# Optimization experiments

Hardware: AMD Instinct MI355X
Metric: run time of the kernel (lower is better)

Reference implementation:

```python
import jax, jax.numpy as jnp
import numpy as np

EPS = 1e-5
L = 8      # n_layers
H = 1024   # n_hidden
F_IN = 26  # input features
B = 65536  # batch


def layer_norm(x, gamma, beta):
    m = jnp.mean(x, axis=-1, keepdims=True)
    v = jnp.mean((x - m) ** 2, axis=-1, keepdims=True)
    return (x - m) * jax.lax.rsqrt(v + EPS) * gamma + beta


def setup_inputs() -> dict:
    key = jax.random.key(0)
    ks = jax.random.split(key, 12)
    s_in = 1.0 / np.sqrt(F_IN)
    s_h = 1.0 / np.sqrt(H)
    return {
        "x": jax.random.normal(ks[0], (B, F_IN), jnp.float32),
        "st_gamma": jnp.ones((F_IN,), jnp.float32),
        "st_beta": jnp.zeros((F_IN,), jnp.float32),
        "st_w": jax.random.uniform(ks[1], (H, F_IN), jnp.float32, -s_in, s_in),
        "st_b": jax.random.uniform(ks[2], (H,), jnp.float32, -s_in, s_in),
        "blk_gamma": jnp.ones((L, H), jnp.float32),
        "blk_beta": jnp.zeros((L, H), jnp.float32),
        "blk_w": jax.random.uniform(ks[3], (L, H, H), jnp.float32, -s_h, s_h),
        "blk_b": jax.random.uniform(ks[4], (L, H), jnp.float32, -s_h, s_h),
        "last_gamma": jnp.ones((H,), jnp.float32),
        "last_beta": jnp.zeros((H,), jnp.float32),
        "last_w": jax.random.uniform(ks[5], (1, H), jnp.float32, -s_h, s_h),
        "last_b": jax.random.uniform(ks[6], (1,), jnp.float32, -s_h, s_h),
    }


def reference(x, st_gamma, st_beta, st_w, st_b,
              blk_gamma, blk_beta, blk_w, blk_b,
              last_gamma, last_beta, last_w, last_b):
    # Stem: LN(26) -> Linear(26->H) -> ReLU (dropout = identity in eval)
    h = jax.nn.relu(layer_norm(x, st_gamma, st_beta) @ st_w.T + st_b)

    # n_layers blocks: LN -> Linear(H->H) -> ReLU, scanned over stacked params
    def body(h, params):
        g, b, w, bb = params
        h = jax.nn.relu(layer_norm(h, g, b) @ w.T + bb)
        return h, None

    h, _ = jax.lax.scan(body, h, (blk_gamma, blk_beta, blk_w, blk_b))

    # Head: LN -> Linear(H->1) -> sigmoid
    h = layer_norm(h, last_gamma, last_beta)
    out = jax.nn.sigmoid(h @ last_w.T + last_b)  # [B, 1]
    return out
```

## Files before the change

kernel.cpp:

```cpp
#include <hip/hip_runtime.h>
#include <hip/hip_bf16.h>
#include <stdint.h>


typedef __attribute__((ext_vector_type(8))) _Float16 f16x8;
typedef __attribute__((ext_vector_type(4))) float f32x4;

#define EPSLN 1e-5f
#define HDIM 1024

__device__ __forceinline__ void gload16(const void* g, void* l) {
  __builtin_amdgcn_global_load_lds(
      (const __attribute__((address_space(1))) unsigned int*)g,
      (__attribute__((address_space(3))) unsigned int*)l, 16, 0, 0);
}

__global__ __launch_bounds__(256) void zero_f32(float* __restrict__ p, int n) {
  int i = blockIdx.x * 256 + threadIdx.x;
  if (i < n) p[i] = 0.f;
}

__global__ __launch_bounds__(256) void fold_blk(
    const float* __restrict__ bg, const float* __restrict__ bb,
    const float* __restrict__ bw, const float* __restrict__ bbias,
    _Float16* __restrict__ Wf, float* __restrict__ bfold, float* __restrict__ Sfold) {
  int lo = blockIdx.x;
  int layer = lo >> 10;
  const float* wrow = bw + (size_t)lo * HDIM;
  const float* g = bg + (size_t)layer * HDIM;
  const float* be = bb + (size_t)layer * HDIM;
  _Float16* wout = Wf + (size_t)lo * HDIM;
  int t = threadIdx.x;
  float s = 0.f, acb = 0.f;
  for (int i = t; i < HDIM; i += 256) {
    float wv = wrow[i];
    _Float16 wp = (_Float16)(wv * g[i]);
    wout[i] = wp;
    s += (float)wp;
    acb += be[i] * wv;
  }
#pragma unroll
  for (int off = 1; off < 64; off <<= 1) { s += __shfl_xor(s, off); acb += __shfl_xor(acb, off); }
  __shared__ float rs[4], rb[4];
  int l = t & 63, w = t >> 6;
  if (l == 0) { rs[w] = s; rb[w] = acb; }
  __syncthreads();
  if (t == 0) {
    Sfold[lo] = rs[0] + rs[1] + rs[2] + rs[3];
    bfold[lo] = bbias[lo] + rb[0] + rb[1] + rb[2] + rb[3];
  }
}

__global__ __launch_bounds__(256) void fold_head(
    const float* __restrict__ lg, const float* __restrict__ lb,
    const float* __restrict__ lw, const float* __restrict__ lbias,
    float* __restrict__ headW, float* __restrict__ headAux) {
  int t = threadIdx.x;
  float s = 0.f, acb = 0.f;
  for (int i = t; i < HDIM; i += 256) {
    float wp = lw[i] * lg[i];
    headW[i] = wp;
    s += wp;
    acb += lb[i] * lw[i];
  }
#pragma unroll
  for (int off = 1; off < 64; off <<= 1) { s += __shfl_xor(s, off); acb += __shfl_xor(acb, off); }
  __shared__ float rs[4], rb[4];
  int l = t & 63, w = t >> 6;
  if (l == 0) { rs[w] = s; rb[w] = acb; }
  __syncthreads();
  if (t == 0) {
    headAux[0] = rs[0] + rs[1] + rs[2] + rs[3];
    headAux[1] = lbias[0] + rb[0] + rb[1] + rb[2] + rb[3];
  }
}

__global__ __launch_bounds__(256) void fold_stem(const float* __restrict__ stw,
                                                 _Float16* __restrict__ Wst) {
  int idx = blockIdx.x * 256 + threadIdx.x;
  int o = idx >> 6, j = idx & 63;
  int i = (((j >> 3) ^ (o & 7)) << 3) + (j & 7);
  Wst[idx] = (i < 26) ? (_Float16)stw[o * 26 + i] : (_Float16)0.f;
}

__global__ __launch_bounds__(256) void stem_gemm(
    const float* __restrict__ x, const float* __restrict__ stg, const float* __restrict__ stb,
    const _Float16* __restrict__ Wst, const float* __restrict__ stbias,
    _Float16* __restrict__ hout, float* __restrict__ stats_out, int rowBase) {
  __shared__ float xin[128 * 26];
  __shared__ _Float16 As[128 * 64];
  __shared__ _Float16 Bs[128 * 64];
  const int t = threadIdx.x;
  const int l = t & 63;
  const int w = t >> 6;
  const int wm = w >> 1, wn = w & 1;
  const int brow = blockIdx.x * 128;
  const int bcol = blockIdx.y * 128;

  const _Float16* gb = Wst + (size_t)(bcol + (t >> 3)) * 64 + (t & 7) * 8;
  char* lB = (char*)Bs + (size_t)w * 1024;
#pragma unroll
  for (int q = 0; q < 4; ++q) gload16(gb + (size_t)q * 32 * 64, lB + q * 4096);

  const float* src = x + ((size_t)rowBase + brow) * 26;
  for (int i = t; i < 128 * 26; i += 256) xin[i] = src[i];
  __syncthreads();

  if (t < 128) {
    float m = 0.f;
#pragma unroll
    for (int i = 0; i < 26; ++i) m += xin[t * 26 + i];
    m *= (1.f / 26.f);
    float v = 0.f;
#pragma unroll
    for (int i = 0; i < 26; ++i) { float d = xin[t * 26 + i] - m; v += d * d; }
    float rstd = rsqrtf(v * (1.f / 26.f) + EPSLN);
    _Float16 tmp[32];
#pragma unroll
    for (int i = 0; i < 26; ++i)
      tmp[i] = (_Float16)((xin[t * 26 + i] - m) * rstd * stg[i] + stb[i]);
#pragma unroll
    for (int i = 26; i < 32; ++i) tmp[i] = (_Float16)0.f;
    char* arow = (char*)As + t * 128;
#pragma unroll
    for (int c = 0; c < 4; ++c) {
      f16x8 vv;
#pragma unroll
      for (int j = 0; j < 8; ++j) vv[j] = tmp[c * 8 + j];
      *(f16x8*)(arow + ((c ^ (t & 7)) << 4)) = vv;
    }
    f16x8 vz = (f16x8)(_Float16)0.f;
#pragma unroll
    for (int c = 4; c < 8; ++c) *(f16x8*)(arow + ((c ^ (t & 7)) << 4)) = vz;
  }
  __syncthreads();

  f32x4 acc[4][4];
#pragma unroll
  for (int i = 0; i < 4; ++i)
#pragma unroll
    for (int j = 0; j < 4; ++j) acc[i][j] = (f32x4){0.f, 0.f, 0.f, 0.f};

#pragma unroll
  for (int ks = 0; ks < 2; ++ks) {
    const int cx = ((ks * 4 + (l >> 4)) ^ (l & 7)) << 4;
    f16x8 af[4], bfr[4];
#pragma unroll
    for (int m = 0; m < 4; ++m)
      af[m] = *(const f16x8*)((const char*)As + (wm * 64 + m * 16 + (l & 15)) * 128 + cx);
#pragma unroll
    for (int n = 0; n < 4; ++n)
      bfr[n] = *(const f16x8*)((const char*)Bs + (wn * 64 + n * 16 + (l & 15)) * 128 + cx);
#pragma unroll
    for (int m = 0; m < 4; ++m)
#pragma unroll
      for (int n = 0; n < 4; ++n)
        acc[m][n] = __builtin_amdgcn_mfma_f32_16x16x32_f16(af[m], bfr[n], acc[m][n], 0, 0, 0);
  }

  __syncthreads();
  float* sred = (float*)xin;
  if (t < 256) sred[t] = 0.f;
  __syncthreads();

  float Bf[4];
#pragma unroll
  for (int n = 0; n < 4; ++n) Bf[n] = stbias[bcol + wn * 64 + n * 16 + (l & 15)];
#pragma unroll
  for (int m = 0; m < 4; ++m) {
#pragma unroll
    for (int rg = 0; rg < 4; ++rg) {
      int rloc = wm * 64 + m * 16 + (l >> 4) * 4 + rg;
      int lrow = brow + rloc;
      float ps = 0.f, psq = 0.f;
#pragma unroll
      for (int n = 0; n < 4; ++n) {
        int col = bcol + wn * 64 + n * 16 + (l & 15);
        float vv = fmaxf(acc[m][n][rg] + Bf[n], 0.f);
        hout[(size_t)lrow * HDIM + col] = (_Float16)vv;
        ps += vv; psq += vv * vv;
      }
#pragma unroll
      for (int off = 1; off < 16; off <<= 1) {
        ps += __shfl_xor(ps, off);
        psq += __shfl_xor(psq, off);
      }
      if ((l & 15) == 0) {
        atomicAdd(&sred[rloc * 2 + 0], ps);
        atomicAdd(&sred[rloc * 2 + 1], psq);
      }
    }
  }
  __syncthreads();
  if (t < 256) atomicAdd(&stats_out[(size_t)(brow + (t >> 1)) * 2 + (t & 1)], sred[t]);
}

__global__ __launch_bounds__(512, 2) void layer_gemm(
    const _Float16* __restrict__ hin, const float* __restrict__ stats_in,
    const _Float16* __restrict__ W, const float* __restrict__ bfold,
    const float* __restrict__ Sfold, _Float16* __restrict__ hout,
    float* __restrict__ stats_out) {
  __shared__ __align__(128) char smem[4 * 32768];
  const int t = threadIdx.x;
  const int l = t & 63;
  const int w = t >> 6;
  const int wm = w >> 2, wn = w & 3;
  int bid = blockIdx.x;
  {
    int nb = gridDim.x;
    if ((nb & 7) == 0) { int cpx = nb >> 3; bid = (bid & 7) * cpx + (bid >> 3); }
  }
  const int brow = (bid >> 2) * 256;
  const int bcol = (bid & 3) * 256;

  f32x4 acc[8][4];
#pragma unroll
  for (int i = 0; i < 8; ++i)
#pragma unroll
    for (int j = 0; j < 4; ++j) acc[i][j] = (f32x4){0.f, 0.f, 0.f, 0.f};

  const int cswz = (t & 3) ^ ((t >> 3) & 3);
  const _Float16* gA = hin + (size_t)(brow + (t >> 2)) * HDIM + cswz * 8;
  const _Float16* gB = W + (size_t)(bcol + (t >> 2)) * HDIM + cswz * 8;
  const int dstw = w << 10;

  auto stage = [&](int kt) {
    char* dA = smem + (kt & 3) * 32768 + dstw;
    const _Float16* sA = gA + kt * 32;
    const _Float16* sB = gB + kt * 32;
    gload16(sA, dA);
    gload16(sA + (size_t)128 * HDIM, dA + 8192);
    gload16(sB, dA + 16384);
    gload16(sB + (size_t)128 * HDIM, dA + 24576);
  };

  const int cxk = (((l >> 4) ^ (((l & 15) >> 1) & 3)) << 4);
  const int arow0 = wm * 8192 + (l & 15) * 64 + cxk;
  const int brow0 = 16384 + wn * 4096 + (l & 15) * 64 + cxk;

  auto tile = [&](int kt, bool do_stage) {
    const char* bc = smem + (kt & 3) * 32768;
    f16x8 bf[4], af[8];
#pragma unroll
    for (int n = 0; n < 4; ++n) bf[n] = *(const f16x8*)(bc + brow0 + n * 1024);
#pragma unroll
    for (int m = 0; m < 8; ++m) af[m] = *(const f16x8*)(bc + arow0 + m * 1024);
    if (do_stage) stage(kt + 3);
    __builtin_amdgcn_s_setprio(1);
#pragma unroll
    for (int m = 0; m < 8; ++m)
#pragma unroll
      for (int n = 0; n < 4; ++n)
        acc[m][n] = __builtin_amdgcn_mfma_f32_16x16x32_f16(af[m], bf[n], acc[m][n], 0, 0, 0);
    __builtin_amdgcn_s_setprio(0);
  };

#define TILE_BARRIER(N)                                      \
  do {                                                       \
    __builtin_amdgcn_sched_barrier(0);                       \
    asm volatile("s_waitcnt vmcnt(" #N ")" ::: "memory");    \
    __builtin_amdgcn_s_barrier();                            \
    __builtin_amdgcn_sched_barrier(0);                       \
  } while (0)

  stage(0);
  stage(1);
  stage(2);
  TILE_BARRIER(8);

#pragma unroll 1
  for (int kt = 0; kt < 29; ++kt) {
    tile(kt, true);
    TILE_BARRIER(8);
  }
  tile(29, false);
  TILE_BARRIER(4);
  tile(30, false);
  TILE_BARRIER(0);
  tile(31, false);
  __syncthreads();
#undef TILE_BARRIER

  float* sred = (float*)smem;
  sred[t] = 0.f;
  __syncthreads();

  float Sf[4], Bf2[4];
#pragma unroll
  for (int n = 0; n < 4; ++n) {
    int col = bcol + wn * 64 + n * 16 + (l & 15);
    Sf[n] = Sfold[col];
    Bf2[n] = bfold[col];
  }
#pragma unroll
  for (int m = 0; m < 8; ++m) {
#pragma unroll
    for (int rg = 0; rg < 4; ++rg) {
      int rloc = wm * 128 + m * 16 + (l >> 4) * 4 + rg;
      int grow = brow + rloc;
      float sum = stats_in[(size_t)grow * 2 + 0];
      float sumsq = stats_in[(size_t)grow * 2 + 1];
      float mean = sum * (1.f / 1024.f);
      float rstd = rsqrtf(sumsq * (1.f / 1024.f) - mean * mean + EPSLN);
      float ps = 0.f, psq = 0.f;
#pragma unroll
      for (int n = 0; n < 4; ++n) {
        int col = bcol + wn * 64 + n * 16 + (l & 15);
        float vv = rstd * (acc[m][n][rg] - mean * Sf[n]) + Bf2[n];
        vv = fmaxf(vv, 0.f);
        hout[(size_t)grow * HDIM + col] = (_Float16)vv;
        ps += vv; psq += vv * vv;
      }
#pragma unroll
      for (int off2 = 1; off2 < 16; off2 <<= 1) {
        ps += __shfl_xor(ps, off2);
        psq += __shfl_xor(psq, off2);
      }
      if ((l & 15) == 0) {
        atomicAdd(&sred[rloc * 2 + 0], ps);
        atomicAdd(&sred[rloc * 2 + 1], psq);
      }
    }
  }
  __syncthreads();
  atomicAdd(&stats_out[(size_t)(brow + (t >> 1)) * 2 + (t & 1)], sred[t]);
}

__global__ __launch_bounds__(512) void head_kernel(
    const _Float16* __restrict__ h8, const float* __restrict__ stats8,
    const float* __restrict__ headW, const float* __restrict__ headAux,
    float* __restrict__ out, int rowBase) {
  int t = threadIdx.x, l = t & 63, w = t >> 6;
  int lrow = blockIdx.x * 8 + w;
  const f16x8* hp = (const f16x8*)(h8 + (size_t)lrow * HDIM) + l * 2;
  f16x8 v0 = hp[0], v1 = hp[1];
  float acc = 0.f;
#pragma unroll
  for (int j = 0; j < 8; ++j) acc += (float)v0[j] * headW[l * 16 + j];
#pragma unroll
  for (int j = 0; j < 8; ++j) acc += (float)v1[j] * headW[l * 16 + 8 + j];
#pragma unroll
  for (int off = 1; off < 64; off <<= 1) acc += __shfl_xor(acc, off);
  if (l == 0) {
    float sum = stats8[lrow * 2 + 0], sumsq = stats8[lrow * 2 + 1];
    float mean = sum * (1.f / 1024.f);
    float rstd = rsqrtf(sumsq * (1.f / 1024.f) - mean * mean + EPSLN);
    float z = rstd * (acc - mean * headAux[0]) + headAux[1];
    out[rowBase + lrow] = 1.f / (1.f + expf(-z));
  }
}

extern "C" void kernel_launch(void* const* d_in, const int* in_sizes, int n_in,
                              void* d_out, int out_size, void* d_ws, size_t ws_size,
                              hipStream_t stream) {
  const float* x      = (const float*)d_in[0];
  const float* stg    = (const float*)d_in[1];
  const float* stb    = (const float*)d_in[2];
  const float* stw    = (const float*)d_in[3];
  const float* stbias = (const float*)d_in[4];
  const float* bg     = (const float*)d_in[5];
  const float* bb     = (const float*)d_in[6];
  const float* bw     = (const float*)d_in[7];
  const float* bbias  = (const float*)d_in[8];
  const float* lg     = (const float*)d_in[9];
  const float* lb     = (const float*)d_in[10];
  const float* lw     = (const float*)d_in[11];
  const float* lbias  = (const float*)d_in[12];
  float* out = (float*)d_out;
  const int B = 65536;
  const int L = 8;

  char* ws = (char*)d_ws;
  size_t off = 0;
  auto carve = [&](size_t bytes) -> char* {
    char* p = ws + off;
    off = (off + bytes + 255) & ~(size_t)255;
    return p;
  };
  _Float16* Wf   = (_Float16*)carve((size_t)L * HDIM * HDIM * 2);
  float* bfold   = (float*)carve((size_t)L * HDIM * 4);
  float* Sfold   = (float*)carve((size_t)L * HDIM * 4);
  float* headW   = (float*)carve((size_t)HDIM * 4);
  float* headAux = (float*)carve(256);
  _Float16* Wst  = (_Float16*)carve((size_t)HDIM * 64 * 2);
  size_t fixed = off;

  int R = B;
  while (R > 256) {
    size_t need = fixed + 2 * ((size_t)R * HDIM * 2 + 256) + ((size_t)9 * R * 2 * 4 + 256);
    if (need <= ws_size) break;
    R >>= 1;
  }
  _Float16* hA = (_Float16*)carve((size_t)R * HDIM * 2);
  _Float16* hB = (_Float16*)carve((size_t)R * HDIM * 2);
  float* stats = (float*)carve((size_t)9 * R * 2 * 4);

  fold_blk<<<L * HDIM, 256, 0, stream>>>(bg, bb, bw, bbias, Wf, bfold, Sfold);
  fold_head<<<1, 256, 0, stream>>>(lg, lb, lw, lbias, headW, headAux);
  fold_stem<<<HDIM * 64 / 256, 256, 0, stream>>>(stw, Wst);

  const int nstats = 9 * R * 2;
  for (int c = 0; c < B / R; ++c) {
    int rowBase = c * R;
    zero_f32<<<(nstats + 255) / 256, 256, 0, stream>>>(stats, nstats);
    {
      dim3 grid(R / 128, 8);
      stem_gemm<<<grid, 256, 0, stream>>>(x, stg, stb, Wst, stbias, hA, stats, rowBase);
    }
    _Float16* cur = hA;
    _Float16* nxt = hB;
    for (int lyr = 0; lyr < L; ++lyr) {
      int nb = (R / 256) * 4;
      layer_gemm<<<nb, 512, 0, stream>>>(
          cur, stats + (size_t)lyr * R * 2, Wf + (size_t)lyr * HDIM * HDIM,
          bfold + lyr * HDIM, Sfold + lyr * HDIM, nxt, stats + (size_t)(lyr + 1) * R * 2);
      _Float16* tmp = cur; cur = nxt; nxt = tmp;
    }
    head_kernel<<<R / 8, 512, 0, stream>>>(cur, stats + (size_t)8 * R * 2, headW, headAux, out, rowBase);
  }
}
```

Before: 1.396 ms.

## Switch layer GEMM to double-buffered K=64 tiles with four-phase staged loads

The main fp16 GEMM loop now uses two 64 KB LDS buffers holding K=64 slices instead of four 32 KB buffers of K=32, halving the number of outer iterations and full barriers. Each tile is split into four MFMA phases separated by barriers, and the global-to-LDS loads for tile kt+2 are interleaved between phases as each sub-region of the buffer is freed. The LDS swizzle is widened to 8 chunks for the 128-byte rows. This aims to overlap memory with MFMA more finely and cut barrier overhead, at the cost of a shallower prefetch distance and more intra-tile barriers.

```diff
diff --git a/kernel.cpp b/kernel.cpp
--- a/kernel.cpp
+++ b/kernel.cpp
@@ -200,7 +200,7 @@
     const _Float16* __restrict__ W, const float* __restrict__ bfold,
     const float* __restrict__ Sfold, _Float16* __restrict__ hout,
     float* __restrict__ stats_out) {
-  __shared__ __align__(128) char smem[4 * 32768];
+  __shared__ __align__(128) char smem[2 * 65536];
   const int t = threadIdx.x;
   const int l = t & 63;
   const int w = t >> 6;
@@ -219,67 +219,138 @@
 #pragma unroll
     for (int j = 0; j < 4; ++j) acc[i][j] = (f32x4){0.f, 0.f, 0.f, 0.f};
 
-  const int cswz = (t & 3) ^ ((t >> 3) & 3);
-  const _Float16* gA = hin + (size_t)(brow + (t >> 2)) * HDIM + cswz * 8;
-  const _Float16* gB = W + (size_t)(bcol + (t >> 2)) * HDIM + cswz * 8;
+  const int cswz = (t & 7) ^ ((t >> 3) & 7);
+  const _Float16* gA = hin + (size_t)(brow + (t >> 3)) * HDIM + cswz * 8;
+  const _Float16* gB = W + (size_t)(bcol + (t >> 3)) * HDIM + cswz * 8;
   const int dstw = w << 10;
 
-  auto stage = [&](int kt) {
-    char* dA = smem + (kt & 3) * 32768 + dstw;
-    const _Float16* sA = gA + kt * 32;
-    const _Float16* sB = gB + kt * 32;
-    gload16(sA, dA);
-    gload16(sA + (size_t)128 * HDIM, dA + 8192);
-    gload16(sB, dA + 16384);
-    gload16(sB + (size_t)128 * HDIM, dA + 24576);
-  };
-
-  const int cxk = (((l >> 4) ^ (((l & 15) >> 1) & 3)) << 4);
-  const int arow0 = wm * 8192 + (l & 15) * 64 + cxk;
-  const int brow0 = 16384 + wn * 4096 + (l & 15) * 64 + cxk;
-
-  auto tile = [&](int kt, bool do_stage) {
-    const char* bc = smem + (kt & 3) * 32768;
-    f16x8 bf[4], af[8];
-#pragma unroll
-    for (int n = 0; n < 4; ++n) bf[n] = *(const f16x8*)(bc + brow0 + n * 1024);
-#pragma unroll
-    for (int m = 0; m < 8; ++m) af[m] = *(const f16x8*)(bc + arow0 + m * 1024);
-    if (do_stage) stage(kt + 3);
+  auto stA0 = [&](int kt) {
+    char* d = smem + (kt & 1) * 65536 + dstw;
+    const _Float16* s = gA + kt * 64;
+    gload16(s, d);
+    gload16(s + (size_t)128 * HDIM, d + 16384);
+  };
+  auto stA1 = [&](int kt) {
+    char* d = smem + (kt & 1) * 65536 + 8192 + dstw;
+    const _Float16* s = gA + kt * 64;
+    gload16(s + (size_t)64 * HDIM, d);
+    gload16(s + (size_t)192 * HDIM, d + 16384);
+  };
+  auto stB0 = [&](int kt) {
+    char* d = smem + (kt & 1) * 65536 + 32768 + dstw;
+    const _Float16* s = gB + kt * 64;
+    gload16(s, d);
+    gload16(s + (size_t)64 * HDIM, d + 8192);
+  };
+  auto stB1 = [&](int kt) {
+    char* d = smem + (kt & 1) * 65536 + 32768 + 16384 + dstw;
+    const _Float16* s = gB + kt * 64;
+    gload16(s + (size_t)128 * HDIM, d);
+    gload16(s + (size_t)192 * HDIM, d + 8192);
+  };
+
+  const int rl = l & 15;
+  const int abase = (wm * 128 + rl) * 128;
+  const int bbase = 32768 + (wn * 64 + rl) * 128;
+  const int cx0 = (((l >> 4) ^ (l & 7)) << 4);
+  const int cx1 = (((4 | (l >> 4)) ^ (l & 7)) << 4);
+
+#define PHASE_BAR()                     \
+  do {                                  \
+    __builtin_amdgcn_sched_barrier(0);  \
+    __builtin_amdgcn_s_barrier();       \
+    __builtin_amdgcn_sched_barrier(0);  \
+  } while (0)
+#define TILE_BOUND(N)                                      \
+  do {                                                     \
+    __builtin_amdgcn_sched_barrier(0);                     \
+    asm volatile("s_waitcnt vmcnt(" #N ")" ::: "memory");  \
+    __builtin_amdgcn_s_barrier();                          \
+    __builtin_amdgcn_sched_barrier(0);                     \
+  } while (0)
+
+  auto tile = [&](int kt, bool st) {
+    const char* bc = smem + (kt & 1) * 65536;
+    f16x8 af[4][2], bf[4][2];
+#pragma unroll
+    for (int n = 0; n < 2; ++n) {
+      bf[n][0] = *(const f16x8*)(bc + bbase + n * 2048 + cx0);
+      bf[n][1] = *(const f16x8*)(bc + bbase + n * 2048 + cx1);
+    }
+#pragma unroll
+    for (int m = 0; m < 4; ++m) {
+      af[m][0] = *(const f16x8*)(bc + abase + m * 2048 + cx0);
+      af[m][1] = *(const f16x8*)(bc + abase + m * 2048 + cx1);
+    }
     __builtin_amdgcn_s_setprio(1);
 #pragma unroll
-    for (int m = 0; m < 8; ++m)
-#pragma unroll
-      for (int n = 0; n < 4; ++n)
-        acc[m][n] = __builtin_amdgcn_mfma_f32_16x16x32_f16(af[m], bf[n], acc[m][n], 0, 0, 0);
+    for (int m = 0; m < 4; ++m)
+#pragma unroll
+      for (int n = 0; n < 2; ++n) {
+        acc[m][n] = __builtin_amdgcn_mfma_f32_16x16x32_f16(af[m][0], bf[n][0], acc[m][n], 0, 0, 0);
+        acc[m][n] = __builtin_amdgcn_mfma_f32_16x16x32_f16(af[m][1], bf[n][1], acc[m][n], 0, 0, 0);
+      }
     __builtin_amdgcn_s_setprio(0);
-  };
-
-#define TILE_BARRIER(N)                                      \
-  do {                                                       \
-    __builtin_amdgcn_sched_barrier(0);                       \
-    asm volatile("s_waitcnt vmcnt(" #N ")" ::: "memory");    \
-    __builtin_amdgcn_s_barrier();                            \
-    __builtin_amdgcn_sched_barrier(0);                       \
-  } while (0)
-
-  stage(0);
-  stage(1);
-  stage(2);
-  TILE_BARRIER(8);
+    PHASE_BAR();
+#pragma unroll
+    for (int n = 2; n < 4; ++n) {
+      bf[n][0] = *(const f16x8*)(bc + bbase + n * 2048 + cx0);
+      bf[n][1] = *(const f16x8*)(bc + bbase + n * 2048 + cx1);
+    }
+    if (st) stA0(kt + 2);
+    __builtin_amdgcn_s_setprio(1);
+#pragma unroll
+    for (int m = 0; m < 4; ++m)
+#pragma unroll
+      for (int n = 2; n < 4; ++n) {
+        acc[m][n] = __builtin_amdgcn_mfma_f32_16x16x32_f16(af[m][0], bf[n][0], acc[m][n], 0, 0, 0);
+        acc[m][n] = __builtin_amdgcn_mfma_f32_16x16x32_f16(af[m][1], bf[n][1], acc[m][n], 0, 0, 0);
+      }
+    __builtin_amdgcn_s_setprio(0);
+    PHASE_BAR();
+#pragma unroll
+    for (int j = 0; j < 4; ++j) {
+      af[j][0] = *(const f16x8*)(bc + abase + (4 + j) * 2048 + cx0);
+      af[j][1] = *(const f16x8*)(bc + abase + (4 + j) * 2048 + cx1);
+    }
+    if (st) stB0(kt + 2);
+    __builtin_amdgcn_s_setprio(1);
+#pragma unroll
+    for (int j = 0; j < 4; ++j)
+#pragma unroll
+      for (int n = 0; n < 2; ++n) {
+        acc[4 + j][n] = __builtin_amdgcn_mfma_f32_16x16x32_f16(af[j][0], bf[n][0], acc[4 + j][n], 0, 0, 0);
+        acc[4 + j][n] = __builtin_amdgcn_mfma_f32_16x16x32_f16(af[j][1], bf[n][1], acc[4 + j][n], 0, 0, 0);
+      }
+    __builtin_amdgcn_s_setprio(0);
+    PHASE_BAR();
+    if (st) { stB1(kt + 2); stA1(kt + 2); }
+    __builtin_amdgcn_s_setprio(1);
+#pragma unroll
+    for (int j = 0; j < 4; ++j)
+#pragma unroll
+      for (int n = 2; n < 4; ++n) {
+        acc[4 + j][n] = __builtin_amdgcn_mfma_f32_16x16x32_f16(af[j][0], bf[n][0], acc[4 + j][n], 0, 0, 0);
+        acc[4 + j][n] = __builtin_amdgcn_mfma_f32_16x16x32_f16(af[j][1], bf[n][1], acc[4 + j][n], 0, 0, 0);
+      }
+    __builtin_amdgcn_s_setprio(0);
+  };
+
+  stA0(0); stA1(0); stB0(0); stB1(0);
+  stA0(1); stA1(1); stB0(1); stB1(1);
+  TILE_BOUND(8);
 
 #pragma unroll 1
-  for (int kt = 0; kt < 29; ++kt) {
+  for (int kt = 0; kt < 14; ++kt) {
     tile(kt, true);
-    TILE_BARRIER(8);
-  }
-  tile(29, false);
-  TILE_BARRIER(4);
-  tile(30, false);
-  TILE_BARRIER(0);
-  tile(31, false);
-  __syncthreads();
-#undef TILE_BARRIER
+    TILE_BOUND(8);
+  }
+  tile(14, false);
+  TILE_BOUND(0);
+  tile(15, false);
+  __syncthreads();
+#undef PHASE_BAR
+#undef TILE_BOUND
 
   float* sred = (float*)smem;
   sred[t] = 0.f;
```

Measured after the change: 1.357 ms. 2.8% less time.

## Shrink layer GEMM block tile to 128x256 with double-buffered LDS

Applied to the files above, without the earlier changes.

Changes the layer GEMM from 512-thread blocks computing 256x256 tiles with a 4-deep LDS pipeline to 256-thread blocks computing 128x256 tiles with 2 LDS buffers. The next K-slice is issued at the start of each tile, and each tile ends with a full vmcnt(0) wait and a barrier. The intent is less LDS per block and more blocks in flight, for better occupancy and scheduling. In exchange, each weight tile is reused across half as many rows, and only one K-step of prefetch hides global-load latency.

```diff
diff --git a/kernel.cpp b/kernel.cpp
--- a/kernel.cpp
+++ b/kernel.cpp
@@ -195,22 +195,22 @@
   if (t < 256) atomicAdd(&stats_out[(size_t)(brow + (t >> 1)) * 2 + (t & 1)], sred[t]);
 }
 
-__global__ __launch_bounds__(512, 2) void layer_gemm(
+__global__ __launch_bounds__(256, 2) void layer_gemm(
     const _Float16* __restrict__ hin, const float* __restrict__ stats_in,
     const _Float16* __restrict__ W, const float* __restrict__ bfold,
     const float* __restrict__ Sfold, _Float16* __restrict__ hout,
     float* __restrict__ stats_out) {
-  __shared__ __align__(128) char smem[4 * 32768];
+  __shared__ __align__(128) char smem[2 * 24576];
   const int t = threadIdx.x;
   const int l = t & 63;
   const int w = t >> 6;
-  const int wm = w >> 2, wn = w & 3;
+  const int wn = w;
   int bid = blockIdx.x;
   {
     int nb = gridDim.x;
     if ((nb & 7) == 0) { int cpx = nb >> 3; bid = (bid & 7) * cpx + (bid >> 3); }
   }
-  const int brow = (bid >> 2) * 256;
+  const int brow = (bid >> 2) * 128;
   const int bcol = (bid & 3) * 256;
 
   f32x4 acc[8][4];
@@ -225,27 +225,40 @@
   const int dstw = w << 10;
 
   auto stage = [&](int kt) {
-    char* dA = smem + (kt & 3) * 32768 + dstw;
+    char* base = smem + (kt & 1) * 24576;
+    char* dA = base + dstw;
+    char* dB = base + 8192 + dstw;
     const _Float16* sA = gA + kt * 32;
     const _Float16* sB = gB + kt * 32;
     gload16(sA, dA);
-    gload16(sA + (size_t)128 * HDIM, dA + 8192);
-    gload16(sB, dA + 16384);
-    gload16(sB + (size_t)128 * HDIM, dA + 24576);
+    gload16(sA + (size_t)64 * HDIM, dA + 4096);
+    gload16(sB, dB);
+    gload16(sB + (size_t)64 * HDIM, dB + 4096);
+    gload16(sB + (size_t)128 * HDIM, dB + 8192);
+    gload16(sB + (size_t)192 * HDIM, dB + 12288);
   };
 
-  const int cxk = (((l >> 4) ^ (((l & 15) >> 1) & 3)) << 4);
-  const int arow0 = wm * 8192 + (l & 15) * 64 + cxk;
-  const int brow0 = 16384 + wn * 4096 + (l & 15) * 64 + cxk;
-
-  auto tile = [&](int kt, bool do_stage) {
-    const char* bc = smem + (kt & 3) * 32768;
+  const int rl = l & 15;
+  const int cx = (((l >> 4) ^ ((rl >> 1) & 3)) << 4);
+  const int arow0 = rl * 64 + cx;
+  const int brow0 = 8192 + (wn * 64 + rl) * 64 + cx;
+
+#define TILE_END()                                   \
+  do {                                               \
+    __builtin_amdgcn_sched_barrier(0);               \
+    asm volatile("s_waitcnt vmcnt(0)" ::: "memory"); \
+    __builtin_amdgcn_s_barrier();                    \
+    __builtin_amdgcn_sched_barrier(0);               \
+  } while (0)
+
+  auto tile = [&](int kt, bool st) {
+    if (st) stage(kt + 1);
+    const char* bc = smem + (kt & 1) * 24576;
     f16x8 bf[4], af[8];
 #pragma unroll
     for (int n = 0; n < 4; ++n) bf[n] = *(const f16x8*)(bc + brow0 + n * 1024);
 #pragma unroll
     for (int m = 0; m < 8; ++m) af[m] = *(const f16x8*)(bc + arow0 + m * 1024);
-    if (do_stage) stage(kt + 3);
     __builtin_amdgcn_s_setprio(1);
 #pragma unroll
     for (int m = 0; m < 8; ++m)
@@ -253,33 +266,16 @@
       for (int n = 0; n < 4; ++n)
         acc[m][n] = __builtin_amdgcn_mfma_f32_16x16x32_f16(af[m], bf[n], acc[m][n], 0, 0, 0);
     __builtin_amdgcn_s_setprio(0);
+    TILE_END();
   };
 
-#define TILE_BARRIER(N)                                      \
-  do {                                                       \
-    __builtin_amdgcn_sched_barrier(0);                       \
-    asm volatile("s_waitcnt vmcnt(" #N ")" ::: "memory");    \
-    __builtin_amdgcn_s_barrier();                            \
-    __builtin_amdgcn_sched_barrier(0);                       \
-  } while (0)
-
   stage(0);
-  stage(1);
-  stage(2);
-  TILE_BARRIER(8);
+  TILE_END();
 
 #pragma unroll 1
-  for (int kt = 0; kt < 29; ++kt) {
-    tile(kt, true);
-    TILE_BARRIER(8);
-  }
-  tile(29, false);
-  TILE_BARRIER(4);
-  tile(30, false);
-  TILE_BARRIER(0);
+  for (int kt = 0; kt < 31; ++kt) tile(kt, true);
   tile(31, false);
-  __syncthreads();
-#undef TILE_BARRIER
+#undef TILE_END
 
   float* sred = (float*)smem;
   sred[t] = 0.f;
@@ -288,7 +284,7 @@
   float Sf[4], Bf2[4];
 #pragma unroll
   for (int n = 0; n < 4; ++n) {
-    int col = bcol + wn * 64 + n * 16 + (l & 15);
+    int col = bcol + wn * 64 + n * 16 + rl;
     Sf[n] = Sfold[col];
     Bf2[n] = bfold[col];
   }
@@ -296,7 +292,7 @@
   for (int m = 0; m < 8; ++m) {
 #pragma unroll
     for (int rg = 0; rg < 4; ++rg) {
-      int rloc = wm * 128 + m * 16 + (l >> 4) * 4 + rg;
+      int rloc = m * 16 + (l >> 4) * 4 + rg;
       int grow = brow + rloc;
       float sum = stats_in[(size_t)grow * 2 + 0];
       float sumsq = stats_in[(size_t)grow * 2 + 1];
@@ -305,7 +301,7 @@
       float ps = 0.f, psq = 0.f;
 #pragma unroll
       for (int n = 0; n < 4; ++n) {
-        int col = bcol + wn * 64 + n * 16 + (l & 15);
+        int col = bcol + wn * 64 + n * 16 + rl;
         float vv = rstd * (acc[m][n][rg] - mean * Sf[n]) + Bf2[n];
         vv = fmaxf(vv, 0.f);
         hout[(size_t)grow * HDIM + col] = (_Float16)vv;
@@ -316,7 +312,7 @@
         ps += __shfl_xor(ps, off2);
         psq += __shfl_xor(psq, off2);
       }
-      if ((l & 15) == 0) {
+      if (rl == 0) {
         atomicAdd(&sred[rloc * 2 + 0], ps);
         atomicAdd(&sred[rloc * 2 + 1], psq);
       }
@@ -410,8 +406,8 @@
     _Float16* cur = hA;
     _Float16* nxt = hB;
     for (int lyr = 0; lyr < L; ++lyr) {
-      int nb = (R / 256) * 4;
-      layer_gemm<<<nb, 512, 0, stream>>>(
+      int nb = (R / 128) * 4;
+      layer_gemm<<<nb, 256, 0, stream>>>(
           cur, stats + (size_t)lyr * R * 2, Wf + (size_t)lyr * HDIM * HDIM,
           bfold + lyr * HDIM, Sfold + lyr * HDIM, nxt, stats + (size_t)(lyr + 1) * R * 2);
       _Float16* tmp = cur; cur = nxt; nxt = tmp;
```

Result: slower. 1.481 ms (+6.1%).
